# Optimization experiments

Hardware: AMD Instinct MI355X
Metric: run time of the kernel (lower is better)

The kernel has to match this reference:

```python
import jax, jax.numpy as jnp
import numpy as np

C_RED = 8
BN_EPS = 1e-5
NORM_EPS = 1e-6

# pairwise upper-triangular index lists (static, matches torch buffers)
_idx_i, _idx_j = [], []
for _i in range(C_RED):
    for _j in range(_i, C_RED):
        _idx_i.append(_i)
        _idx_j.append(_j)
IDX_I = np.array(_idx_i, dtype=np.int32)
IDX_J = np.array(_idx_j, dtype=np.int32)


def setup_inputs() -> dict:
    key = jax.random.key(0)
    ks = jax.random.split(key, 8)
    B, Cin, H, W = 32, 256, 56, 56
    x = jax.random.normal(ks[0], (B, Cin, H, W), dtype=jnp.float32)
    w_reduce = jax.random.normal(ks[1], (C_RED, Cin, 1, 1), dtype=jnp.float32) * 0.05
    bn_gamma = jax.random.uniform(ks[2], (C_RED,), dtype=jnp.float32, minval=0.5, maxval=1.5)
    bn_beta = jax.random.normal(ks[3], (C_RED,), dtype=jnp.float32) * 0.1
    bn_mean = jax.random.normal(ks[4], (C_RED,), dtype=jnp.float32) * 0.1
    bn_var = jax.random.uniform(ks[5], (C_RED,), dtype=jnp.float32, minval=0.5, maxval=1.5)
    w_dw = jax.random.normal(ks[6], (C_RED, 1, 3, 3), dtype=jnp.float32) * 0.3
    scale = jax.random.uniform(ks[7], (1, C_RED, 1, 1), dtype=jnp.float32, minval=0.5, maxval=1.5)
    return {"x": x, "w_reduce": w_reduce, "bn_gamma": bn_gamma, "bn_beta": bn_beta,
            "bn_mean": bn_mean, "bn_var": bn_var, "w_dw": w_dw, "scale": scale}


def _l2norm_ch(z):
    # F.normalize(p=2, dim=1, eps=1e-6): x / max(||x||_2, eps)
    n = jnp.sqrt(jnp.sum(z * z, axis=1, keepdims=True))
    return z / jnp.maximum(n, NORM_EPS)


def reference(x, w_reduce, bn_gamma, bn_beta, bn_mean, bn_var, w_dw, scale):
    # 1x1 conv (no bias)
    z = jax.lax.conv_general_dilated(x, w_reduce, (1, 1), 'VALID',
                                     dimension_numbers=('NCHW', 'OIHW', 'NCHW'))
    # BatchNorm (inference) + ReLU
    inv = bn_gamma / jnp.sqrt(bn_var + BN_EPS)
    z = z * inv[None, :, None, None] + (bn_beta - bn_mean * inv)[None, :, None, None]
    z = jax.nn.relu(z)
    # depthwise 3x3 twist conv, padding 1, times per-channel scale
    z_twist = jax.lax.conv_general_dilated(z, w_dw, (1, 1), ((1, 1), (1, 1)),
                                           dimension_numbers=('NCHW', 'OIHW', 'NCHW'),
                                           feature_group_count=C_RED) * scale
    z_norm = _l2norm_ch(z)
    z_twist_norm = _l2norm_ch(z_twist)
    # gathered pairwise products over upper-triangular channel pairs
    interactions = jnp.take(z_norm, IDX_I, axis=1) * jnp.take(z_twist_norm, IDX_J, axis=1)
    return jnp.concatenate([z_norm, interactions], axis=1)  # [B, 8+36, H, W]
```

## Files before the change

### kernel.cpp

```cpp
#include <hip/hip_runtime.h>

#define BATCH 32
#define CIN   256
#define CR    8
#define HDIM  56
#define WDIM  56
#define HW    3136
#define COUT  44

__global__ __launch_bounds__(256) void k1_reduce_bn_relu(
    const float* __restrict__ x, const float* __restrict__ wr,
    const float* __restrict__ gamma, const float* __restrict__ beta,
    const float* __restrict__ mean, const float* __restrict__ var,
    float* __restrict__ z)
{
    const int t = blockIdx.x * 256 + threadIdx.x;
    const int b = t / HW;
    const int p = t - b * HW;
    const float* xp = x + (size_t)b * CIN * HW + p;

    float acc[CR];
#pragma unroll
    for (int c = 0; c < CR; ++c) acc[c] = 0.f;

#pragma unroll 32
    for (int cin = 0; cin < CIN; ++cin) {
        const float xv = __builtin_nontemporal_load(xp + (size_t)cin * HW);
#pragma unroll
        for (int c = 0; c < CR; ++c)
            acc[c] = fmaf(xv, wr[c * CIN + cin], acc[c]);
    }

    float v[CR];
#pragma unroll
    for (int c = 0; c < CR; ++c) {
        const float inv = gamma[c] / sqrtf(var[c] + 1e-5f);
        const float sh  = beta[c] - mean[c] * inv;
        v[c] = fmaxf(fmaf(acc[c], inv, sh), 0.f);
    }

    float4* zp = reinterpret_cast<float4*>(z + (size_t)t * CR);
    zp[0] = make_float4(v[0], v[1], v[2], v[3]);
    zp[1] = make_float4(v[4], v[5], v[6], v[7]);
}

__global__ __launch_bounds__(256) void k2_dw_norm_inter(
    const float* __restrict__ z, const float* __restrict__ wdw,
    const float* __restrict__ scale, float* __restrict__ out)
{
    const int t = blockIdx.x * 256 + threadIdx.x;
    const int b = t / HW;
    const int p = t - b * HW;
    const int h = p / WDIM;
    const int w = p - h * WDIM;

    const float4 c0 = reinterpret_cast<const float4*>(z + (size_t)t * CR)[0];
    const float4 c1 = reinterpret_cast<const float4*>(z + (size_t)t * CR)[1];
    const float zc[CR] = {c0.x, c0.y, c0.z, c0.w, c1.x, c1.y, c1.z, c1.w};

    float tw[CR];
#pragma unroll
    for (int c = 0; c < CR; ++c) tw[c] = 0.f;

#pragma unroll
    for (int dy = -1; dy <= 1; ++dy) {
        const int hh = h + dy;
        const bool okh = (hh >= 0) && (hh < HDIM);
#pragma unroll
        for (int dx = -1; dx <= 1; ++dx) {
            const int ww = w + dx;
            const bool ok = okh && (ww >= 0) && (ww < WDIM);
            if (ok) {
                const float* zn = z + ((size_t)(b * HW + hh * WDIM + ww)) * CR;
                const float4 n0 = reinterpret_cast<const float4*>(zn)[0];
                const float4 n1 = reinterpret_cast<const float4*>(zn)[1];
                const float nv[CR] = {n0.x, n0.y, n0.z, n0.w, n1.x, n1.y, n1.z, n1.w};
                const int k = (dy + 1) * 3 + (dx + 1);
#pragma unroll
                for (int c = 0; c < CR; ++c)
                    tw[c] = fmaf(nv[c], wdw[c * 9 + k], tw[c]);
            }
        }
    }

    float s1 = 0.f, s2 = 0.f;
#pragma unroll
    for (int c = 0; c < CR; ++c) {
        tw[c] *= scale[c];
        s1 = fmaf(zc[c], zc[c], s1);
        s2 = fmaf(tw[c], tw[c], s2);
    }
    const float r1 = 1.0f / fmaxf(sqrtf(s1), 1e-6f);
    const float r2 = 1.0f / fmaxf(sqrtf(s2), 1e-6f);

    float a[CR], tb[CR];
#pragma unroll
    for (int c = 0; c < CR; ++c) { a[c] = zc[c] * r1; tb[c] = tw[c] * r2; }

    float* op = out + (size_t)b * COUT * HW + p;
#pragma unroll
    for (int c = 0; c < CR; ++c)
        __builtin_nontemporal_store(a[c], op + (size_t)c * HW);

    int idx = CR;
#pragma unroll
    for (int i = 0; i < CR; ++i) {
#pragma unroll
        for (int j = i; j < CR; ++j) {
            __builtin_nontemporal_store(a[i] * tb[j], op + (size_t)idx * HW);
            ++idx;
        }
    }
}

extern "C" void kernel_launch(void* const* d_in, const int* in_sizes, int n_in,
                              void* d_out, int out_size, void* d_ws, size_t ws_size,
                              hipStream_t stream) {
    const float* x     = (const float*)d_in[0];
    const float* wr    = (const float*)d_in[1];
    const float* gamma = (const float*)d_in[2];
    const float* beta  = (const float*)d_in[3];
    const float* mean  = (const float*)d_in[4];
    const float* var   = (const float*)d_in[5];
    const float* wdw   = (const float*)d_in[6];
    const float* scale = (const float*)d_in[7];
    float* out = (float*)d_out;
    float* z   = (float*)d_ws;

    const int npix = BATCH * HW;
    k1_reduce_bn_relu<<<npix / 256, 256, 0, stream>>>(x, wr, gamma, beta, mean, var, z);
    k2_dw_norm_inter<<<npix / 256, 256, 0, stream>>>(z, wdw, scale, out);
}
```

Before: 190.6 us.

## Split 1x1 reduction over input channels across warps with LDS reduction

```diff
diff --git a/kernel.cpp b/kernel.cpp
--- a/kernel.cpp
+++ b/kernel.cpp
@@ -14,41 +14,51 @@
     const float* __restrict__ mean, const float* __restrict__ var,
     float* __restrict__ z)
 {
-    const int t = blockIdx.x * 256 + threadIdx.x;
-    const int b = t / HW;
-    const int p = t - b * HW;
-    const float* xp = x + (size_t)b * CIN * HW + p;
+    __shared__ float part[4][CR][64];
+
+    const int lane  = threadIdx.x & 63;
+    const int slice = threadIdx.x >> 6;
+    const int base  = blockIdx.x * 64;
+    const int t     = base + lane;
+    const int b     = t / HW;
+    const int p     = t - b * HW;
+    const float* xp = x + (size_t)b * CIN * HW + p + (size_t)(slice * 64) * HW;
+    const float* wp = wr + slice * 64;
 
     float acc[CR];
 #pragma unroll
     for (int c = 0; c < CR; ++c) acc[c] = 0.f;
 
 #pragma unroll 32
-    for (int cin = 0; cin < CIN; ++cin) {
+    for (int cin = 0; cin < 64; ++cin) {
         const float xv = __builtin_nontemporal_load(xp + (size_t)cin * HW);
 #pragma unroll
         for (int c = 0; c < CR; ++c)
-            acc[c] = fmaf(xv, wr[c * CIN + cin], acc[c]);
+            acc[c] = fmaf(xv, wp[c * CIN + cin], acc[c]);
     }
 
-    float v[CR];
 #pragma unroll
-    for (int c = 0; c < CR; ++c) {
-        const float inv = gamma[c] / sqrtf(var[c] + 1e-5f);
-        const float sh  = beta[c] - mean[c] * inv;
-        v[c] = fmaxf(fmaf(acc[c], inv, sh), 0.f);
+    for (int c = 0; c < CR; ++c) part[slice][c][lane] = acc[c];
+    __syncthreads();
+
+#pragma unroll
+    for (int half = 0; half < 2; ++half) {
+        const int v  = threadIdx.x + half * 256;
+        const int px = v >> 3;
+        const int ch = v & 7;
+        const float sum = part[0][ch][px] + part[1][ch][px]
+                        + part[2][ch][px] + part[3][ch][px];
+        const float inv = gamma[ch] / sqrtf(var[ch] + 1e-5f);
+        const float sh  = beta[ch] - mean[ch] * inv;
+        z[(size_t)base * CR + v] = fmaxf(fmaf(sum, inv, sh), 0.f);
     }
-
-    float4* zp = reinterpret_cast<float4*>(z + (size_t)t * CR);
-    zp[0] = make_float4(v[0], v[1], v[2], v[3]);
-    zp[1] = make_float4(v[4], v[5], v[6], v[7]);
 }
 
-__global__ __launch_bounds__(256) void k2_dw_norm_inter(
+__global__ __launch_bounds__(64) void k2_dw_norm_inter(
     const float* __restrict__ z, const float* __restrict__ wdw,
     const float* __restrict__ scale, float* __restrict__ out)
 {
-    const int t = blockIdx.x * 256 + threadIdx.x;
+    const int t = blockIdx.x * 64 + threadIdx.x;
     const int b = t / HW;
     const int p = t - b * HW;
     const int h = p / WDIM;
@@ -128,6 +138,6 @@
     float* z   = (float*)d_ws;
 
     const int npix = BATCH * HW;
-    k1_reduce_bn_relu<<<npix / 256, 256, 0, stream>>>(x, wr, gamma, beta, mean, var, z);
-    k2_dw_norm_inter<<<npix / 256, 256, 0, stream>>>(z, wdw, scale, out);
+    k1_reduce_bn_relu<<<npix / 64, 256, 0, stream>>>(x, wr, gamma, beta, mean, var, z);
+    k2_dw_norm_inter<<<npix / 64, 64, 0, stream>>>(z, wdw, scale, out);
 }
```

Result: faster. 184.0 us (-3.5%).
